# Kernel tuning notes

Measured on AMD Instinct MI355X. Metric: run time of the kernel, lower is better.

The kernel has to match this reference:

```python
import jax, jax.numpy as jnp
import numpy as np

B, K, C, HEADS, R, N, FF = 8, 512, 256, 8, 4, 64, 1024
HT = 2 * R + 1  # rel-pos table side = 9


def layer_norm(x, g, b, eps=1e-5):
    mu = jnp.mean(x, axis=-1, keepdims=True)
    var = jnp.var(x, axis=-1, keepdims=True)
    return (x - mu) * jax.lax.rsqrt(var + eps) * g + b


def grid_sample_table(table, grid):
    """Bilinear grid_sample, align_corners=True, zeros padding.
    table: [heads, H, W] (batch-expanded in torch, identical per batch)
    grid:  [b, k, n, 2] in [-1, 1]  ->  out [b, heads, k, n]
    """
    heads, H, W = table.shape
    gx = (grid[..., 0] + 1.0) * 0.5 * (W - 1)
    gy = (grid[..., 1] + 1.0) * 0.5 * (H - 1)
    x0 = jnp.floor(gx); y0 = jnp.floor(gy)
    x1 = x0 + 1.0;      y1 = y0 + 1.0
    wx1 = gx - x0; wx0 = 1.0 - wx1
    wy1 = gy - y0; wy0 = 1.0 - wy1
    flat = table.reshape(heads, H * W)

    def corner(yi, xi, w):
        valid = (xi >= 0) & (xi <= W - 1) & (yi >= 0) & (yi <= H - 1)
        idx = (jnp.clip(yi, 0, H - 1) * W + jnp.clip(xi, 0, W - 1)).astype(jnp.int32)
        return flat[:, idx] * jnp.where(valid, w, 0.0)[None]  # [heads,b,k,n]

    out = (corner(y0, x0, wy0 * wx0) + corner(y0, x1, wy0 * wx1)
           + corner(y1, x0, wy1 * wx0) + corner(y1, x1, wy1 * wx1))
    return jnp.moveaxis(out, 0, 1)  # [b, heads, k, n]


def setup_inputs() -> dict:
    key = jax.random.key(0)
    ks = jax.random.split(key, 16)
    s = 1.0 / np.sqrt(C)
    inp = {
        "query": jax.random.normal(ks[0], (B, K, C), jnp.float32),
        "local_feat": jax.random.normal(ks[1], (B, C, K, N), jnp.float32),
        "local_spat": jax.random.uniform(ks[2], (B, K, N, 2), jnp.float32) * 2.0 - 1.0,
        # rel-pos table is zeros-initialized in torch; use small randn so it's non-trivial
        "rel_table": jax.random.normal(ks[3], (HEADS, HT, HT), jnp.float32) * 0.02,
        "Wq": jax.random.normal(ks[4], (C, C), jnp.float32) * s,
        "bq": jnp.zeros((C,), jnp.float32),
        "Wk": jax.random.normal(ks[5], (C, C), jnp.float32) * s,
        "bk": jnp.zeros((C,), jnp.float32),
        "Wv": jax.random.normal(ks[6], (C, C), jnp.float32) * s,
        "bv": jnp.zeros((C,), jnp.float32),
        "Wo": jax.random.normal(ks[7], (C, C), jnp.float32) * s,
        "bo": jnp.zeros((C,), jnp.float32),
        "ln1_g": jnp.ones((C,), jnp.float32),
        "ln1_b": jnp.zeros((C,), jnp.float32),
        "W1": jax.random.normal(ks[8], (C, FF), jnp.float32) * s,
        "b1": jnp.zeros((FF,), jnp.float32),
        "W2": jax.random.normal(ks[9], (FF, C), jnp.float32) * (1.0 / np.sqrt(FF)),
        "b2": jnp.zeros((C,), jnp.float32),
        "ln2_g": jnp.ones((C,), jnp.float32),
        "ln2_b": jnp.zeros((C,), jnp.float32),
    }
    return inp


def reference(query, local_feat, local_spat, rel_table, Wq, bq, Wk, bk, Wv, bv,
              Wo, bo, ln1_g, ln1_b, W1, b1, W2, b2, ln2_g, ln2_b):
    b, k, c = query.shape
    heads = rel_table.shape[0]
    d = c // heads
    n = local_feat.shape[-1]
    # spatial_score: grid_sample of rel-pos table at per-key offsets -> attention bias
    bias = grid_sample_table(rel_table, local_spat)      # [b, heads, k, n]
    bias = jnp.transpose(bias, (0, 2, 1, 3))             # [b, k, heads, n]
    # local bilateral attention (query attends to its n local samples)
    q = (query @ Wq + bq).reshape(b, k, heads, d)
    feats = jnp.transpose(local_feat, (0, 2, 3, 1))      # [b, k, n, c]
    Kp = (feats @ Wk + bk).reshape(b, k, n, heads, d)
    Vp = (feats @ Wv + bv).reshape(b, k, n, heads, d)
    scores = jnp.einsum('bkhd,bknhd->bkhn', q, Kp) / jnp.sqrt(jnp.float32(d)) + bias
    attn = jax.nn.softmax(scores, axis=-1)
    ctx = jnp.einsum('bkhn,bknhd->bkhd', attn, Vp).reshape(b, k, c)
    x = layer_norm(query + ctx @ Wo + bo, ln1_g, ln1_b)
    h = jax.nn.gelu(x @ W1 + b1) @ W2 + b2
    out = layer_norm(x + h, ln2_g, ln2_b)
    # num_local_scales == 1: stack+mean over scales is identity
    return out
```

## Files before the change

### kernel.cpp

```cpp
#include <hip/hip_runtime.h>
#include <hip/hip_bf16.h>

typedef __hip_bfloat16 bf16;
typedef __attribute__((ext_vector_type(8))) short short8;
typedef __attribute__((ext_vector_type(4))) float float4_;

#define DEV static __device__ __forceinline__

DEV float blo(unsigned w){ return __uint_as_float(w << 16); }
DEV float bhi(unsigned w){ return __uint_as_float(w & 0xffff0000u); }
DEV unsigned short f2bu(float x){ bf16 h = __float2bfloat16(x); unsigned short u; __builtin_memcpy(&u, &h, 2); return u; }
DEV unsigned pack2(float a, float b){ return (unsigned)f2bu(a) | ((unsigned)f2bu(b) << 16); }

DEV float gelu_tanh(float x){
  float z = 0.7978845608028654f * (x + 0.044715f * x * x * x);
  float th = 2.0f / (1.0f + __expf(-2.0f * z)) - 1.0f;
  return 0.5f * x * (1.0f + th);
}


__global__ __launch_bounds__(256) void k_prep(
    const float* __restrict__ query, const float* __restrict__ Wq,
    const float* __restrict__ Wk, const float* __restrict__ Wv,
    const float* __restrict__ Wo, const float* __restrict__ W1, const float* __restrict__ W2,
    bf16* __restrict__ query_bf, bf16* __restrict__ WqT, bf16* __restrict__ WkP,
    bf16* __restrict__ WvP, bf16* __restrict__ WoT, bf16* __restrict__ W1T, bf16* __restrict__ W2T)
{
  __shared__ ushort ts[64][72];
  const int t = threadIdx.x;
  const int bx = blockIdx.x;

  if (bx < 160){
    const float* src; bf16* dst; int ldi, ldo, kt, nt;
    if (bx < 16)      { src = Wq; dst = WqT; ldi = 256;  ldo = 256;  kt = bx & 3;        nt = bx >> 2; }
    else if (bx < 32) { src = Wo; dst = WoT; ldi = 256;  ldo = 256;  kt = (bx-16) & 3;   nt = (bx-16) >> 2; }
    else if (bx < 96) { src = W1; dst = W1T; ldi = 1024; ldo = 256;  kt = (bx-32) & 3;   nt = (bx-32) >> 2; }
    else              { src = W2; dst = W2T; ldi = 256;  ldo = 1024; kt = (bx-96) & 15;  nt = (bx-96) >> 4; }
    int k0 = kt * 64, n0 = nt * 64;
    {
      int r = t >> 2, c0 = (t & 3) * 16;
      #pragma unroll
      for (int g = 0; g < 4; g++){
        float4 v = *(const float4*)&src[(size_t)(k0 + r)*ldi + n0 + c0 + g*4];
        ts[r][c0+g*4+0] = f2bu(v.x); ts[r][c0+g*4+1] = f2bu(v.y);
        ts[r][c0+g*4+2] = f2bu(v.z); ts[r][c0+g*4+3] = f2bu(v.w);
      }
    }
    __syncthreads();
    {
      int rr = t >> 2, cc0 = (t & 3) * 16;
      unsigned wbuf[8];
      #pragma unroll
      for (int j = 0; j < 8; j++)
        wbuf[j] = (unsigned)ts[cc0+2*j][rr] | ((unsigned)ts[cc0+2*j+1][rr] << 16);
      uint4* d = (uint4*)(dst + (size_t)(n0 + rr)*ldo + k0 + cc0);
      d[0] = make_uint4(wbuf[0], wbuf[1], wbuf[2], wbuf[3]);
      d[1] = make_uint4(wbuf[4], wbuf[5], wbuf[6], wbuf[7]);
    }
  } else if (bx < 192){
    int idx = bx - 160, h = idx >> 2, kt = idx & 3, k0 = kt * 64;
    {
      int r = t >> 2, d0 = (t & 3) * 8;
      #pragma unroll
      for (int g = 0; g < 2; g++){
        float4 v = *(const float4*)&Wv[(size_t)(k0 + r)*256 + h*32 + d0 + g*4];
        ts[r][d0+g*4+0] = f2bu(v.x); ts[r][d0+g*4+1] = f2bu(v.y);
        ts[r][d0+g*4+2] = f2bu(v.z); ts[r][d0+g*4+3] = f2bu(v.w);
      }
    }
    __syncthreads();
    {
      int d = t >> 3, cc0 = (t & 7) * 8;
      unsigned wbuf[4];
      #pragma unroll
      for (int j = 0; j < 4; j++)
        wbuf[j] = (unsigned)ts[cc0+2*j][d] | ((unsigned)ts[cc0+2*j+1][d] << 16);
      *(uint4*)(WvP + (size_t)h*8192 + (size_t)d*256 + k0 + cc0) =
          make_uint4(wbuf[0], wbuf[1], wbuf[2], wbuf[3]);
    }
  } else if (bx < 200){
    int off = (bx - 192) * 8192;
    #pragma unroll
    for (int g = 0; g < 8; g++){
      int i = off + g*1024 + t*4;
      int h = i >> 13, c = (i >> 5) & 255, d = i & 31;
      float4 v = *(const float4*)&Wk[(size_t)c*256 + h*32 + d];
      *(uint2*)(WkP + i) = make_uint2(pack2(v.x, v.y), pack2(v.z, v.w));
    }
  } else {
    int off = (bx - 200) * 16384;
    #pragma unroll
    for (int g = 0; g < 16; g++){
      int i = off + g*1024 + t*4;
      float4 v = *(const float4*)&query[i];
      *(uint2*)(query_bf + i) = make_uint2(pack2(v.x, v.y), pack2(v.z, v.w));
    }
  }
}

template<int KDIM, int NT, int EPI>
__global__ __launch_bounds__(256) void k_gemm(
    const bf16* __restrict__ A, int lda, int acolH,
    const bf16* __restrict__ BT, int btH,
    const float* __restrict__ bias,
    bf16* __restrict__ Cb, int ldc, int ncolH)
{
  constexpr int KB = (KDIM >= 64) ? 64 : 32;
  constexpr int LP = KB + 8;
  constexpr int ASEG = KB / 8;
  __shared__ short As[64][LP];
  __shared__ short Bs[NT][LP];

  const int t = threadIdx.x;
  const int w = t >> 6, l = t & 63, lm = l & 15, lq = l >> 4;
  const int m0 = blockIdx.x * 64;
  const int h = blockIdx.z;
  const size_t acol = (size_t)h * acolH;
  const bf16* Bt = BT + (size_t)h * btH + (size_t)(blockIdx.y * NT) * KDIM;
  const int ncol = h * ncolH + blockIdx.y * NT;

  float4_ acc[NT/16];
  #pragma unroll
  for (int i = 0; i < NT/16; i++) acc[i] = (float4_){0.f,0.f,0.f,0.f};

  for (int k0 = 0; k0 < KDIM; k0 += KB){
    if (k0) __syncthreads();
    for (int i = t; i < 64*ASEG; i += 256){
      int row = i / ASEG, seg = i % ASEG;
      uint4 v = *(const uint4*)(A + (size_t)(m0+row)*lda + acol + k0 + seg*8);
      *(uint4*)&As[row][seg*8] = v;
    }
    for (int i = t; i < NT*ASEG; i += 256){
      int row = i / ASEG, seg = i % ASEG;
      uint4 v = *(const uint4*)(Bt + (size_t)row*KDIM + k0 + seg*8);
      *(uint4*)&Bs[row][seg*8] = v;
    }
    __syncthreads();
    #pragma unroll
    for (int kk = 0; kk < KB/32; kk++){
      short8 af = *(const short8*)&As[w*16 + lm][kk*32 + lq*8];
      #pragma unroll
      for (int nt = 0; nt < NT/16; nt++){
        short8 bfr = *(const short8*)&Bs[nt*16 + lm][kk*32 + lq*8];
        acc[nt] = __builtin_amdgcn_mfma_f32_16x16x32_bf16(af, bfr, acc[nt], 0, 0, 0);
      }
    }
  }

  #pragma unroll
  for (int nt = 0; nt < NT/16; nt++){
    int gcol = ncol + nt*16 + lm;
    float bb = bias ? bias[gcol] : 0.0f;
    #pragma unroll
    for (int rg = 0; rg < 4; rg++){
      int row = m0 + w*16 + lq*4 + rg;
      float v = acc[nt][rg] + bb;
      if (EPI == 0) Cb[(size_t)row*ldc + gcol] = __float2bfloat16(v);
      else          Cb[(size_t)row*ldc + gcol] = __float2bfloat16(gelu_tanh(v));
    }
  }
}

template<int KDIM, int WRITE_BF>
__global__ __launch_bounds__(256) void k_gemm_ln(
    const bf16* __restrict__ A, int lda,
    const bf16* __restrict__ BT,
    const float* __restrict__ bias,
    const float* __restrict__ resid,
    const float* __restrict__ gamma, const float* __restrict__ beta,
    float* __restrict__ Cf, bf16* __restrict__ Cb)
{
  constexpr int KB = 64, LP = 72;
  __shared__ short As[16][LP];
  __shared__ short Bs[256][LP];
  __shared__ float2 part[4][16];

  const int t = threadIdx.x;
  const int w = t >> 6, l = t & 63, lm = l & 15, lq = l >> 4;
  const int m0 = blockIdx.x * 16;

  float4_ acc[4];
  #pragma unroll
  for (int i = 0; i < 4; i++) acc[i] = (float4_){0.f,0.f,0.f,0.f};

  for (int k0 = 0; k0 < KDIM; k0 += KB){
    if (k0) __syncthreads();
    if (t < 128){
      int row = t >> 3, seg = t & 7;
      uint4 v = *(const uint4*)(A + (size_t)(m0+row)*lda + k0 + seg*8);
      *(uint4*)&As[row][seg*8] = v;
    }
    for (int i = t; i < 2048; i += 256){
      int row = i >> 3, seg = i & 7;
      uint4 v = *(const uint4*)(BT + (size_t)row*KDIM + k0 + seg*8);
      *(uint4*)&Bs[row][seg*8] = v;
    }
    __syncthreads();
    #pragma unroll
    for (int kk = 0; kk < 2; kk++){
      short8 af = *(const short8*)&As[lm][kk*32 + lq*8];
      #pragma unroll
      for (int nt = 0; nt < 4; nt++){
        short8 bfr = *(const short8*)&Bs[w*64 + nt*16 + lm][kk*32 + lq*8];
        acc[nt] = __builtin_amdgcn_mfma_f32_16x16x32_bf16(af, bfr, acc[nt], 0, 0, 0);
      }
    }
  }

  float v[4][4];
  float s1[4] = {0,0,0,0}, s2[4] = {0,0,0,0};
  #pragma unroll
  for (int nt = 0; nt < 4; nt++){
    int col = w*64 + nt*16 + lm;
    float bb = bias[col];
    #pragma unroll
    for (int rg = 0; rg < 4; rg++){
      int row = m0 + lq*4 + rg;
      float x = acc[nt][rg] + bb + resid[(size_t)row*256 + col];
      v[nt][rg] = x;
      s1[rg] += x; s2[rg] += x*x;
    }
  }
  #pragma unroll
  for (int off = 1; off < 16; off <<= 1){
    #pragma unroll
    for (int rg = 0; rg < 4; rg++){
      s1[rg] += __shfl_xor(s1[rg], off);
      s2[rg] += __shfl_xor(s2[rg], off);
    }
  }
  if (lm == 0){
    #pragma unroll
    for (int rg = 0; rg < 4; rg++)
      part[w][lq*4 + rg] = make_float2(s1[rg], s2[rg]);
  }
  __syncthreads();
  #pragma unroll
  for (int rg = 0; rg < 4; rg++){
    int rl = lq*4 + rg;
    float S1 = part[0][rl].x + part[1][rl].x + part[2][rl].x + part[3][rl].x;
    float S2 = part[0][rl].y + part[1][rl].y + part[2][rl].y + part[3][rl].y;
    float mean = S1 * (1.0f/256.0f);
    float var  = S2 * (1.0f/256.0f) - mean*mean;
    float inv  = rsqrtf(var + 1e-5f);
    #pragma unroll
    for (int nt = 0; nt < 4; nt++){
      int col = w*64 + nt*16 + lm;
      float o = (v[nt][rg] - mean) * inv * gamma[col] + beta[col];
      size_t idx = (size_t)(m0 + rl)*256 + col;
      Cf[idx] = o;
      if (WRITE_BF) Cb[idx] = __float2bfloat16(o);
    }
  }
}

__global__ __launch_bounds__(256) void k_attn(
    const float* __restrict__ local_feat, const float* __restrict__ local_spat,
    const float* __restrict__ rel_table, const bf16* __restrict__ qk,
    bf16* __restrict__ fctx)
{
  __shared__ ushort fs[256][66];
  __shared__ float qks[8][256];
  __shared__ float attn_t[64][12];
  __shared__ float tab[648];
  __shared__ float bw4[64][4];
  __shared__ int   bix[64][4];

  const int t = threadIdx.x;
  const int r = blockIdx.x;
  const int b = r >> 9, k = r & 511;

  {
    int cb = t >> 2;
    int nq = (t & 3) * 16;
    #pragma unroll
    for (int p = 0; p < 4; p++){
      int c = p * 64 + cb;
      const float4* src = (const float4*)(local_feat + ((size_t)((b*256 + c)*512 + k))*64 + nq);
      unsigned* d = (unsigned*)&fs[c][nq];
      #pragma unroll
      for (int g = 0; g < 4; g++){
        float4 v = src[g];
        d[g*2+0] = pack2(v.x, v.y);
        d[g*2+1] = pack2(v.z, v.w);
      }
    }
  }
  {
    const uint4* src = (const uint4*)(qk + (size_t)r * 2048 + t * 8);
    uint4 a = *src;
    int h = t >> 5, c0 = (t & 31) * 8;
    float* d = &qks[h][c0];
    d[0]=blo(a.x); d[1]=bhi(a.x); d[2]=blo(a.y); d[3]=bhi(a.y);
    d[4]=blo(a.z); d[5]=bhi(a.z); d[6]=blo(a.w); d[7]=bhi(a.w);
  }
  for (int i = t; i < 648; i += 256) tab[i] = rel_table[i];
  if (t < 64){
    int n = t;
    float2 sxy = *(const float2*)&local_spat[((size_t)r*64 + n)*2];
    float gx = (sxy.x + 1.0f) * 4.0f, gy = (sxy.y + 1.0f) * 4.0f;
    float x0f = floorf(gx), y0f = floorf(gy);
    int xi0 = (int)x0f, yi0 = (int)y0f;
    float wx1 = gx - x0f, wx0 = 1.0f - wx1;
    float wy1 = gy - y0f, wy0 = 1.0f - wy1;
    int xs[4] = {xi0, xi0 + 1, xi0, xi0 + 1};
    int ys[4] = {yi0, yi0, yi0 + 1, yi0 + 1};
    float ww[4] = {wy0*wx0, wy0*wx1, wy1*wx0, wy1*wx1};
    #pragma unroll
    for (int j2 = 0; j2 < 4; j2++){
      int xx = xs[j2], yy = ys[j2];
      bool valid = (xx >= 0) && (xx <= 8) && (yy >= 0) && (yy <= 8);
      int xc = min(max(xx, 0), 8), yc = min(max(yy, 0), 8);
      bix[n][j2] = yc * 9 + xc;
      bw4[n][j2] = valid ? ww[j2] : 0.0f;
    }
  }
  __syncthreads();

  {
    int h = t >> 5, n0 = (t & 31) * 2;
    float s0 = 0.f, s1 = 0.f;
    for (int c = 0; c < 256; c += 4){
      float4 qv = *(const float4*)&qks[h][c];
      unsigned w0 = *(const unsigned*)&fs[c+0][n0];
      unsigned w1 = *(const unsigned*)&fs[c+1][n0];
      unsigned w2 = *(const unsigned*)&fs[c+2][n0];
      unsigned w3 = *(const unsigned*)&fs[c+3][n0];
      s0 += qv.x*blo(w0) + qv.y*blo(w1) + qv.z*blo(w2) + qv.w*blo(w3);
      s1 += qv.x*bhi(w0) + qv.y*bhi(w1) + qv.z*bhi(w2) + qv.w*bhi(w3);
    }
    const float scale = 0.17677669529663687f;
    int n1 = n0 + 1;
    float bias0 = tab[h*81 + bix[n0][0]] * bw4[n0][0] + tab[h*81 + bix[n0][1]] * bw4[n0][1]
                + tab[h*81 + bix[n0][2]] * bw4[n0][2] + tab[h*81 + bix[n0][3]] * bw4[n0][3];
    float bias1 = tab[h*81 + bix[n1][0]] * bw4[n1][0] + tab[h*81 + bix[n1][1]] * bw4[n1][1]
                + tab[h*81 + bix[n1][2]] * bw4[n1][2] + tab[h*81 + bix[n1][3]] * bw4[n1][3];
    float sc0 = s0 * scale + bias0;
    float sc1 = s1 * scale + bias1;
    float m = fmaxf(sc0, sc1);
    #pragma unroll
    for (int off = 1; off < 32; off <<= 1) m = fmaxf(m, __shfl_xor(m, off));
    float e0 = __expf(sc0 - m), e1 = __expf(sc1 - m);
    float s = e0 + e1;
    #pragma unroll
    for (int off = 1; off < 32; off <<= 1) s += __shfl_xor(s, off);
    float inv = 1.0f / s;
    attn_t[n0][h] = e0 * inv;
    attn_t[n1][h] = e1 * inv;
  }
  __syncthreads();

  {
    const int c = t;
    float f[8] = {0,0,0,0,0,0,0,0};
    for (int n = 0; n < 64; n += 2){
      unsigned wa = *(const unsigned*)&fs[c][n];
      float a0 = blo(wa), a1 = bhi(wa);
      float4 A0 = *(const float4*)&attn_t[n][0];
      float4 A1 = *(const float4*)&attn_t[n][4];
      float4 B0 = *(const float4*)&attn_t[n+1][0];
      float4 B1 = *(const float4*)&attn_t[n+1][4];
      f[0] += A0.x*a0 + B0.x*a1;  f[1] += A0.y*a0 + B0.y*a1;
      f[2] += A0.z*a0 + B0.z*a1;  f[3] += A0.w*a0 + B0.w*a1;
      f[4] += A1.x*a0 + B1.x*a1;  f[5] += A1.y*a0 + B1.y*a1;
      f[6] += A1.z*a0 + B1.z*a1;  f[7] += A1.w*a0 + B1.w*a1;
    }
    #pragma unroll
    for (int h = 0; h < 8; h++)
      fctx[(size_t)r*2048 + h*256 + c] = __float2bfloat16(f[h]);
  }
}

extern "C" void kernel_launch(void* const* d_in, const int* in_sizes, int n_in,
                              void* d_out, int out_size, void* d_ws, size_t ws_size,
                              hipStream_t stream)
{
  const float* query      = (const float*)d_in[0];
  const float* local_feat = (const float*)d_in[1];
  const float* local_spat = (const float*)d_in[2];
  const float* rel_table  = (const float*)d_in[3];
  const float* Wq  = (const float*)d_in[4];   const float* bq  = (const float*)d_in[5];
  const float* Wk  = (const float*)d_in[6];
  const float* Wv  = (const float*)d_in[8];   const float* bv  = (const float*)d_in[9];
  const float* Wo  = (const float*)d_in[10];  const float* bo  = (const float*)d_in[11];
  const float* g1  = (const float*)d_in[12];  const float* be1 = (const float*)d_in[13];
  const float* W1  = (const float*)d_in[14];  const float* b1  = (const float*)d_in[15];
  const float* W2  = (const float*)d_in[16];  const float* b2  = (const float*)d_in[17];
  const float* g2  = (const float*)d_in[18];  const float* be2 = (const float*)d_in[19];

  char* ws = (char*)d_ws;
  bf16*  qk       = (bf16*)(ws + 0);
  bf16*  fctx     = (bf16*)(ws + 16777216);
  bf16*  query_bf = (bf16*)(ws + 33554432);
  bf16*  q_bf     = (bf16*)(ws + 35651584);
  bf16*  WqT      = (bf16*)(ws + 37748736);
  bf16*  WkP      = (bf16*)(ws + 37879808);
  bf16*  WvP      = (bf16*)(ws + 38010880);
  bf16*  WoT      = (bf16*)(ws + 38141952);
  bf16*  W1T      = (bf16*)(ws + 38273024);
  bf16*  W2T      = (bf16*)(ws + 38797312);
  bf16*  ctx_bf   = (bf16*)(ws + 0);
  float* x        = (float*)(ws + 2097152);
  bf16*  x_bf     = (bf16*)(ws + 6291456);
  bf16*  h1       = (bf16*)(ws + 20971520);
  float* out      = (float*)d_out;

  dim3 blk(256);
  k_prep<<<dim3(264), blk, 0, stream>>>(query, Wq, Wk, Wv, Wo, W1, W2,
                                        query_bf, WqT, WkP, WvP, WoT, W1T, W2T);
  k_gemm<256,64,0><<<dim3(64,4,1), blk, 0, stream>>>(query_bf, 256, 0, WqT, 0, bq, q_bf, 256, 0);
  k_gemm<32,64,0><<<dim3(64,4,8), blk, 0, stream>>>(q_bf, 256, 32, WkP, 8192, nullptr, qk, 2048, 256);
  k_attn<<<dim3(4096), blk, 0, stream>>>(local_feat, local_spat, rel_table, qk, fctx);
  k_gemm<256,32,0><<<dim3(64,1,8), blk, 0, stream>>>(fctx, 2048, 256, WvP, 8192, bv, ctx_bf, 256, 32);
  k_gemm_ln<256,1><<<dim3(256), blk, 0, stream>>>(ctx_bf, 256, WoT, bo, query, g1, be1, x, x_bf);
  k_gemm<256,64,2><<<dim3(64,16,1), blk, 0, stream>>>(x_bf, 256, 0, W1T, 0, b1, h1, 1024, 0);
  k_gemm_ln<1024,0><<<dim3(256), blk, 0, stream>>>(h1, 1024, W2T, b2, x, g2, be2, out, nullptr);
}
```

Before: 523.5 us.

## Use MFMA for attention scores with transposed swizzled feature tile in k_attn

Stores local features transposed in LDS ([n][c], XOR-swizzled) so the q·K score computation runs on bf16 16x16x32 MFMA instructions instead of scalar FMA loops. The rel-pos bias is computed per sample directly from global memory into a per-head LDS array, and the context accumulation is restructured so each thread handles 4 channels × 2 heads with vectorized stores. This removes scalar FMA work in the score phase at the cost of an extra barrier, 16-bit scattered LDS writes during the transpose, and 8 of 16 MFMA columns wasted on duplicated heads.

```diff
diff --git a/kernel.cpp b/kernel.cpp
--- a/kernel.cpp
+++ b/kernel.cpp
@@ -259,45 +259,44 @@
     const float* __restrict__ rel_table, const bf16* __restrict__ qk,
     bf16* __restrict__ fctx)
 {
-  __shared__ ushort fs[256][66];
-  __shared__ float qks[8][256];
+  __shared__ __attribute__((aligned(16))) ushort fsT[64][264];
+  __shared__ __attribute__((aligned(16))) ushort qkb[8][264];
+  __shared__ float biasS[8][68];
+  __shared__ float s_sc[64][10];
   __shared__ float attn_t[64][12];
-  __shared__ float tab[648];
-  __shared__ float bw4[64][4];
-  __shared__ int   bix[64][4];
 
   const int t = threadIdx.x;
   const int r = blockIdx.x;
   const int b = r >> 9, k = r & 511;
+  const int w = t >> 6, l = t & 63, lm = l & 15, lq = l >> 4;
 
   {
     int cb = t >> 2;
     int nq = (t & 3) * 16;
+    int key = (t & 3) << 3;
     #pragma unroll
     for (int p = 0; p < 4; p++){
       int c = p * 64 + cb;
+      int cs = c ^ key;
       const float4* src = (const float4*)(local_feat + ((size_t)((b*256 + c)*512 + k))*64 + nq);
-      unsigned* d = (unsigned*)&fs[c][nq];
       #pragma unroll
       for (int g = 0; g < 4; g++){
         float4 v = src[g];
-        d[g*2+0] = pack2(v.x, v.y);
-        d[g*2+1] = pack2(v.z, v.w);
+        int row = nq + g*4;
+        fsT[row+0][cs] = f2bu(v.x);
+        fsT[row+1][cs] = f2bu(v.y);
+        fsT[row+2][cs] = f2bu(v.z);
+        fsT[row+3][cs] = f2bu(v.w);
       }
     }
   }
   {
-    const uint4* src = (const uint4*)(qk + (size_t)r * 2048 + t * 8);
-    uint4 a = *src;
+    uint4 a = *(const uint4*)(qk + (size_t)r * 2048 + t * 8);
     int h = t >> 5, c0 = (t & 31) * 8;
-    float* d = &qks[h][c0];
-    d[0]=blo(a.x); d[1]=bhi(a.x); d[2]=blo(a.y); d[3]=bhi(a.y);
-    d[4]=blo(a.z); d[5]=bhi(a.z); d[6]=blo(a.w); d[7]=bhi(a.w);
-  }
-  for (int i = t; i < 648; i += 256) tab[i] = rel_table[i];
+    *(uint4*)&qkb[h][c0] = a;
+  }
   if (t < 64){
-    int n = t;
-    float2 sxy = *(const float2*)&local_spat[((size_t)r*64 + n)*2];
+    float2 sxy = *(const float2*)&local_spat[((size_t)r*64 + t)*2];
     float gx = (sxy.x + 1.0f) * 4.0f, gy = (sxy.y + 1.0f) * 4.0f;
     float x0f = floorf(gx), y0f = floorf(gy);
     int xi0 = (int)x0f, yi0 = (int)y0f;
@@ -305,38 +304,45 @@
     float wy1 = gy - y0f, wy0 = 1.0f - wy1;
     int xs[4] = {xi0, xi0 + 1, xi0, xi0 + 1};
     int ys[4] = {yi0, yi0, yi0 + 1, yi0 + 1};
-    float ww[4] = {wy0*wx0, wy0*wx1, wy1*wx0, wy1*wx1};
-    #pragma unroll
-    for (int j2 = 0; j2 < 4; j2++){
-      int xx = xs[j2], yy = ys[j2];
-      bool valid = (xx >= 0) && (xx <= 8) && (yy >= 0) && (yy <= 8);
-      int xc = min(max(xx, 0), 8), yc = min(max(yy, 0), 8);
-      bix[n][j2] = yc * 9 + xc;
-      bw4[n][j2] = valid ? ww[j2] : 0.0f;
+    float wj[4] = {wy0*wx0, wy0*wx1, wy1*wx0, wy1*wx1};
+    float ww[4]; int ix[4];
+    #pragma unroll
+    for (int j = 0; j < 4; j++){
+      bool valid = (xs[j] >= 0) && (xs[j] <= 8) && (ys[j] >= 0) && (ys[j] <= 8);
+      ix[j] = min(max(ys[j],0),8)*9 + min(max(xs[j],0),8);
+      ww[j] = valid ? wj[j] : 0.0f;
+    }
+    #pragma unroll
+    for (int h = 0; h < 8; h++){
+      const float* th = rel_table + h*81;
+      biasS[h][t] = th[ix[0]]*ww[0] + th[ix[1]]*ww[1] + th[ix[2]]*ww[2] + th[ix[3]]*ww[3];
     }
   }
   __syncthreads();
 
   {
-    int h = t >> 5, n0 = (t & 31) * 2;
-    float s0 = 0.f, s1 = 0.f;
-    for (int c = 0; c < 256; c += 4){
-      float4 qv = *(const float4*)&qks[h][c];
-      unsigned w0 = *(const unsigned*)&fs[c+0][n0];
-      unsigned w1 = *(const unsigned*)&fs[c+1][n0];
-      unsigned w2 = *(const unsigned*)&fs[c+2][n0];
-      unsigned w3 = *(const unsigned*)&fs[c+3][n0];
-      s0 += qv.x*blo(w0) + qv.y*blo(w1) + qv.z*blo(w2) + qv.w*blo(w3);
-      s1 += qv.x*bhi(w0) + qv.y*bhi(w1) + qv.z*bhi(w2) + qv.w*bhi(w3);
-    }
-    const float scale = 0.17677669529663687f;
-    int n1 = n0 + 1;
-    float bias0 = tab[h*81 + bix[n0][0]] * bw4[n0][0] + tab[h*81 + bix[n0][1]] * bw4[n0][1]
-                + tab[h*81 + bix[n0][2]] * bw4[n0][2] + tab[h*81 + bix[n0][3]] * bw4[n0][3];
-    float bias1 = tab[h*81 + bix[n1][0]] * bw4[n1][0] + tab[h*81 + bix[n1][1]] * bw4[n1][1]
-                + tab[h*81 + bix[n1][2]] * bw4[n1][2] + tab[h*81 + bix[n1][3]] * bw4[n1][3];
-    float sc0 = s0 * scale + bias0;
-    float sc1 = s1 * scale + bias1;
+    float4_ acc = (float4_){0.f,0.f,0.f,0.f};
+    const int skey = (w & 3) << 3;
+    #pragma unroll
+    for (int ks = 0; ks < 8; ks++){
+      short8 af  = *(const short8*)&fsT[w*16 + lm][(ks*32 + lq*8) ^ skey];
+      short8 bfr = *(const short8*)&qkb[lm & 7][ks*32 + lq*8];
+      acc = __builtin_amdgcn_mfma_f32_16x16x32_bf16(af, bfr, acc, 0, 0, 0);
+    }
+    if (lm < 8){
+      const float scale = 0.17677669529663687f;
+      #pragma unroll
+      for (int rg = 0; rg < 4; rg++){
+        int n = w*16 + lq*4 + rg;
+        s_sc[n][lm] = acc[rg] * scale + biasS[lm][n];
+      }
+    }
+  }
+  __syncthreads();
+
+  {
+    int g = t >> 5, j = t & 31;
+    float sc0 = s_sc[j][g], sc1 = s_sc[j+32][g];
     float m = fmaxf(sc0, sc1);
     #pragma unroll
     for (int off = 1; off < 32; off <<= 1) m = fmaxf(m, __shfl_xor(m, off));
@@ -345,29 +351,27 @@
     #pragma unroll
     for (int off = 1; off < 32; off <<= 1) s += __shfl_xor(s, off);
     float inv = 1.0f / s;
-    attn_t[n0][h] = e0 * inv;
-    attn_t[n1][h] = e1 * inv;
+    attn_t[j][g]    = e0 * inv;
+    attn_t[j+32][g] = e1 * inv;
   }
   __syncthreads();
 
   {
-    const int c = t;
-    float f[8] = {0,0,0,0,0,0,0,0};
-    for (int n = 0; n < 64; n += 2){
-      unsigned wa = *(const unsigned*)&fs[c][n];
-      float a0 = blo(wa), a1 = bhi(wa);
-      float4 A0 = *(const float4*)&attn_t[n][0];
-      float4 A1 = *(const float4*)&attn_t[n][4];
-      float4 B0 = *(const float4*)&attn_t[n+1][0];
-      float4 B1 = *(const float4*)&attn_t[n+1][4];
-      f[0] += A0.x*a0 + B0.x*a1;  f[1] += A0.y*a0 + B0.y*a1;
-      f[2] += A0.z*a0 + B0.z*a1;  f[3] += A0.w*a0 + B0.w*a1;
-      f[4] += A1.x*a0 + B1.x*a1;  f[5] += A1.y*a0 + B1.y*a1;
-      f[6] += A1.z*a0 + B1.z*a1;  f[7] += A1.w*a0 + B1.w*a1;
-    }
-    #pragma unroll
-    for (int h = 0; h < 8; h++)
-      fctx[(size_t)r*2048 + h*256 + c] = __float2bfloat16(f[h]);
+    const int cg = t >> 2, hh = t & 3;
+    const int c0 = cg * 4, h0 = hh * 2;
+    float f0[4] = {0,0,0,0}, f1[4] = {0,0,0,0};
+    #pragma unroll 4
+    for (int n = 0; n < 64; n++){
+      int key = ((n >> 4) & 3) << 3;
+      uint2 wv = *(const uint2*)&fsT[n][c0 ^ key];
+      float a0 = blo(wv.x), a1 = bhi(wv.x), a2 = blo(wv.y), a3 = bhi(wv.y);
+      float2 A = *(const float2*)&attn_t[n][h0];
+      f0[0] += A.x*a0; f0[1] += A.x*a1; f0[2] += A.x*a2; f0[3] += A.x*a3;
+      f1[0] += A.y*a0; f1[1] += A.y*a1; f1[2] += A.y*a2; f1[3] += A.y*a3;
+    }
+    size_t base = (size_t)r*2048 + (size_t)h0*256 + c0;
+    *(uint2*)&fctx[base]       = make_uint2(pack2(f0[0], f0[1]), pack2(f0[2], f0[3]));
+    *(uint2*)&fctx[base + 256] = make_uint2(pack2(f1[0], f1[1]), pack2(f1[2], f1[3]));
   }
 }
 
```

Result: faster. 504.0 us (-3.7%).
